# Performance work log

Measured on AMD Instinct MI355X. Metric: run time of the kernel, lower is better.

The kernel has to match this reference:

```python
import jax, jax.numpy as jnp
import numpy as np

H, D, DIM = 8, 128, 1024   # heads, dim_head, model dim (inner_dim = H*D = DIM)
QB, N = 16, 512            # 'q' and 'n' dims of the [q, n, dim] inputs


def layer_norm(x, g, b, eps=1e-5):
    mu = x.mean(-1, keepdims=True)
    var = ((x - mu) ** 2).mean(-1, keepdims=True)
    return (x - mu) / jnp.sqrt(var + eps) * g + b


def setup_inputs() -> dict:
    key = jax.random.key(0)
    ks = jax.random.split(key, 8)
    rn = lambda k, shape, s=1.0: jax.random.normal(k, shape, jnp.float32) * s
    return {
        'q': rn(ks[0], (QB, N, DIM)),
        'k': rn(ks[1], (QB, N, DIM)),
        'v': rn(ks[2], (QB, N, DIM)),
        'ln_g': jnp.ones(DIM, jnp.float32),
        'ln_b': jnp.zeros(DIM, jnp.float32),
        'w_in': rn(ks[3], (H * D, DIM), 0.02),          # Linear(dim -> inner_dim), no bias
        'wp_w1': rn(ks[4], (D, 2 * D), 0.05),           # weight_predictor Linear(2d -> d)
        'wp_b1': jnp.zeros(D, jnp.float32),
        'wp_ln_g': jnp.ones(D, jnp.float32),
        'wp_ln_b': jnp.zeros(D, jnp.float32),
        'wp_w2': rn(ks[5], (3, D), 0.05),               # Linear(d -> 3)
        'wp_b2': jnp.zeros(3, jnp.float32),
        'w_out': rn(ks[6], (DIM, H * D), 0.02),         # output Linear(inner_dim -> dim)
        'b_out': jnp.zeros(DIM, jnp.float32),
    }


def reference(q, k, v, ln_g, ln_b, w_in, wp_w1, wp_b1, wp_ln_g, wp_ln_b,
              wp_w2, wp_b2, w_out, b_out):
    def proj(t):
        x = layer_norm(t, ln_g, ln_b) @ w_in.T                 # [Q, N, H*D]
        Qd, Nd = t.shape[0], t.shape[1]
        return x.reshape(Qd, Nd, H, D).transpose(2, 0, 1, 3)   # [h, q, n, d]

    f_q, f_k, f_v = proj(q), proj(k), proj(v)

    # cosine similarity component
    dots = jnp.einsum('hqnd,hqmd->hqnm', f_q, f_k)
    qn = jnp.linalg.norm(f_q, axis=-1)                          # [h, q, n]
    kn = jnp.linalg.norm(f_k, axis=-1)                          # [h, q, m]
    cosine_sim = dots / (qn[..., :, None] * kn[..., None, :])

    q_centered = f_q - f_q.mean(-1, keepdims=True)

    # variance component (unbiased variance, clipped ratio vs target_var=1)
    q_var = jnp.var(f_q, axis=-1, ddof=1)
    k_var = jnp.var(f_k, axis=-1, ddof=1)
    q_ratio = 2.0 * jnp.minimum(q_var, 1.0) / (q_var + 1.0)
    k_ratio = 2.0 * jnp.minimum(k_var, 1.0) / (k_var + 1.0)
    var_component = jnp.einsum('hqn,hqm->hqnm', q_ratio, k_ratio)

    # decorrelation-scaled covariance component (overwrites the dead loop in the source)
    q_flat = q_centered.reshape(H, -1, D)                        # [h, q*n, d]
    feat_corr = jnp.einsum('hnd,hne->hde', q_flat, q_flat) / q_flat.shape[1]
    feat_corr = feat_corr * (1.0 - jnp.eye(D, dtype=feat_corr.dtype))
    decorr_score = jnp.linalg.norm(feat_corr, axis=(-2, -1)) / (D * D)
    decorr_scale = jnp.exp(-5.0 * decorr_score)[:, None, None, None]
    cov_component = cosine_sim * decorr_scale

    # dynamic per-head weight mixing
    q_global = f_q.mean(axis=(1, 2))                             # [h, d]
    k_global = f_k.mean(axis=(1, 2))
    feats = jnp.concatenate([q_global, k_global], axis=-1)       # [h, 2d]
    h1 = jnp.maximum(layer_norm(feats @ wp_w1.T + wp_b1, wp_ln_g, wp_ln_b), 0.0)
    weights = jax.nn.softmax(h1 @ wp_w2.T + wp_b2, axis=-1)      # [h, 3]
    cw = weights[:, 0][:, None, None, None]
    vw = weights[:, 1][:, None, None, None]
    ww = weights[:, 2][:, None, None, None]
    mixed = cw * cosine_sim + vw * cov_component + ww * var_component

    out = jnp.einsum('hqnm,hqmd->hqnd', mixed, f_v)
    out = out.transpose(1, 2, 0, 3).reshape(q.shape[0], q.shape[1], H * D)
    return out @ w_out.T + b_out
```

## Files before the change

### kernel.cpp

```cpp
#include <hip/hip_runtime.h>
#include <hip/hip_bf16.h>

typedef unsigned short u16;
typedef __attribute__((ext_vector_type(8))) short short8;
typedef __attribute__((ext_vector_type(4))) float floatx4;

#define H 8
#define D 128
#define DIM 1024
#define QB 16
#define NSEQ 512
#define R 8192

__device__ inline u16 f2b(float x) {
    union { float f; unsigned int u; } c{x};
    unsigned int lsb = (c.u >> 16) & 1;
    unsigned int r = c.u + 0x7fffu + lsb;
    return (u16)(r >> 16);
}
__device__ inline float b2f(u16 u) {
    union { unsigned int i; float f; } c;
    c.i = (unsigned int)u << 16;
    return c.f;
}

#define GLOAD_LDS16(gptr, lptr)                                                        \
    __builtin_amdgcn_global_load_lds(                                                  \
        (const __attribute__((address_space(1))) unsigned int*)(gptr),                 \
        (__attribute__((address_space(3))) unsigned int*)(lptr), 16, 0, 0)

__global__ __launch_bounds__(256) void ln_all(const float* __restrict__ q,
                                              const float* __restrict__ k,
                                              const float* __restrict__ v,
                                              const float* __restrict__ g,
                                              const float* __restrict__ b,
                                              u16* __restrict__ out) {
    const float* src = (blockIdx.y == 0) ? q : (blockIdx.y == 1) ? k : v;
    int r = blockIdx.x;
    int tid = threadIdx.x;
    const float* row = src + (size_t)r * DIM;
    float4 vv = *(const float4*)(row + tid * 4);
    float sum = vv.x + vv.y + vv.z + vv.w;
    float sq = vv.x * vv.x + vv.y * vv.y + vv.z * vv.z + vv.w * vv.w;
    __shared__ float s1[256], s2[256];
    s1[tid] = sum; s2[tid] = sq;
    __syncthreads();
    for (int s = 128; s > 0; s >>= 1) {
        if (tid < s) { s1[tid] += s1[tid + s]; s2[tid] += s2[tid + s]; }
        __syncthreads();
    }
    float mean = s1[0] * (1.0f / DIM);
    float var = s2[0] * (1.0f / DIM) - mean * mean;
    float rstd = rsqrtf(var + 1e-5f);
    float4 gv = *(const float4*)(g + tid * 4);
    float4 bv = *(const float4*)(b + tid * 4);
    ushort4 pk;
    pk.x = f2b((vv.x - mean) * rstd * gv.x + bv.x);
    pk.y = f2b((vv.y - mean) * rstd * gv.y + bv.y);
    pk.z = f2b((vv.z - mean) * rstd * gv.z + bv.z);
    pk.w = f2b((vv.w - mean) * rstd * gv.w + bv.w);
    *(ushort4*)(out + ((size_t)blockIdx.y * R + r) * DIM + tid * 4) = pk;
}

__global__ __launch_bounds__(256) void cvt2_kernel(const float* __restrict__ a,
                                                   const float* __restrict__ b,
                                                   u16* __restrict__ oa,
                                                   u16* __restrict__ ob, int n4each) {
    int i = blockIdx.x * 256 + threadIdx.x;
    const float* src; u16* dst; int j;
    if (i < n4each) { src = a; dst = oa; j = i; }
    else            { src = b; dst = ob; j = i - n4each; }
    float4 v = *(const float4*)(src + (size_t)j * 4);
    ushort4 pk;
    pk.x = f2b(v.x); pk.y = f2b(v.y); pk.z = f2b(v.z); pk.w = f2b(v.w);
    *(ushort4*)(dst + (size_t)j * 4) = pk;
}

__global__ __launch_bounds__(256) void gemm_qkv(const u16* __restrict__ A,
                                                const u16* __restrict__ B,
                                                u16* __restrict__ qT,
                                                u16* __restrict__ fqb,
                                                u16* __restrict__ kTh,
                                                u16* __restrict__ vT,
                                                float* __restrict__ qn,
                                                float* __restrict__ qm,
                                                float* __restrict__ qr,
                                                float* __restrict__ kn,
                                                float* __restrict__ kr) {
    __shared__ u16 smem[19712];
    u16* As = smem;
    u16* Bs = smem + 4096;
    float* sred = (float*)(smem + 18432);
    float* invb = (float*)(smem + 19456);

    const int tid = threadIdx.x;
    const int bb = blockIdx.x;
    const int xcd = bb & 7, j0 = bb >> 3;
    const int h = j0 & 7;
    const int rowblk = xcd * 24 + (j0 >> 3);
    const int m0 = rowblk * 128, n0 = h * 128;
    const int seg = rowblk >> 6;
    const int lrb = (rowblk & 63) * 128;

    const int wave = tid >> 6, lane = tid & 63;
    const int wm = (wave >> 1) * 64, wn = (wave & 1) * 64;
    const int fr = lane & 15, kq = lane >> 4;
    const int srow = tid >> 2, scol = (tid & 3) * 8;

    floatx4 acc[4][4] = {};
    const size_t aOff0 = (size_t)(m0 + srow) * DIM + scol;
    const size_t aOff1 = (size_t)(m0 + 64 + srow) * DIM + scol;
    const size_t bOff0 = (size_t)(n0 + srow) * DIM + scol;
    const size_t bOff1 = (size_t)(n0 + 64 + srow) * DIM + scol;

    for (int kt = 0; kt < DIM; kt += 32) {
        GLOAD_LDS16(A + aOff0 + kt, As + tid * 8);
        GLOAD_LDS16(A + aOff1 + kt, As + (256 + tid) * 8);
        GLOAD_LDS16(B + bOff0 + kt, Bs + tid * 8);
        GLOAD_LDS16(B + bOff1 + kt, Bs + (256 + tid) * 8);
        __syncthreads();
        short8 xf[4], wf[4];
#pragma unroll
        for (int i = 0; i < 4; i++)
            xf[i] = *(const short8*)&As[(wm + i * 16 + fr) * 32 + kq * 8];
#pragma unroll
        for (int j = 0; j < 4; j++)
            wf[j] = *(const short8*)&Bs[(wn + j * 16 + fr) * 32 + kq * 8];
#pragma unroll
        for (int j = 0; j < 4; j++)
#pragma unroll
            for (int i = 0; i < 4; i++)
                acc[j][i] = __builtin_amdgcn_mfma_f32_16x16x32_bf16(wf[j], xf[i], acc[j][i], 0, 0, 0);
        __syncthreads();
    }

    if (seg <= 1) {
        const int half = wn >> 6;
#pragma unroll
        for (int i = 0; i < 4; i++) {
            float s = 0.0f, qs = 0.0f;
#pragma unroll
            for (int j = 0; j < 4; j++)
#pragma unroll
                for (int rg = 0; rg < 4; rg++) {
                    float vv = acc[j][i][rg];
                    s += vv; qs += vv * vv;
                }
            s += __shfl_xor(s, 16); qs += __shfl_xor(qs, 16);
            s += __shfl_xor(s, 32); qs += __shfl_xor(qs, 32);
            if (kq == 0) {
                int rl = wm + i * 16 + fr;
                sred[rl * 4 + half * 2 + 0] = s;
                sred[rl * 4 + half * 2 + 1] = qs;
            }
        }
        __syncthreads();
        if (tid < 128) {
            float sum = sred[tid * 4 + 0] + sred[tid * 4 + 2];
            float sq  = sred[tid * 4 + 1] + sred[tid * 4 + 3];
            float nrm = sqrtf(sq);
            float var = (sq - sum * sum * (1.0f / D)) * (1.0f / (D - 1));
            float ratio = 2.0f * fminf(var, 1.0f) / (var + 1.0f);
            size_t idx = (size_t)h * R + lrb + tid;
            if (seg == 0) {
                qn[idx] = nrm; qm[idx] = sum * (1.0f / D); qr[idx] = ratio;
            } else {
                kn[idx] = nrm; kr[idx] = ratio;
                invb[tid] = 1.0f / nrm;
            }
        }
        __syncthreads();
    }

    u16* dstT = (seg == 0) ? qT : (seg == 1) ? kTh : vT;
#pragma unroll
    for (int i = 0; i < 4; i++) {
        const int rl = wm + i * 16 + fr;
        const float sc = (seg == 1) ? invb[rl] : 1.0f;
#pragma unroll
        for (int j = 0; j < 4; j++) {
#pragma unroll
            for (int rg = 0; rg < 4; rg++) {
                const int cl = wn + j * 16 + kq * 4 + rg;
                dstT[(size_t)(h * D + cl) * R + lrb + rl] = f2b(acc[j][i][rg] * sc);
            }
        }
    }

    if (seg == 0) {
        __syncthreads();
        u16* Tw = smem + wave * 4608;
#pragma unroll
        for (int i = 0; i < 4; i++)
#pragma unroll
            for (int j = 0; j < 4; j++) {
                ushort4 pk;
                pk.x = f2b(acc[j][i][0]); pk.y = f2b(acc[j][i][1]);
                pk.z = f2b(acc[j][i][2]); pk.w = f2b(acc[j][i][3]);
                *(ushort4*)&Tw[(i * 16 + fr) * 72 + j * 16 + kq * 4] = pk;
            }
        __syncthreads();
#pragma unroll
        for (int p = 0; p < 16; p++) {
            int rloc = p * 4 + kq;
            int c4 = fr * 4;
            ushort4 v = *(const ushort4*)&Tw[rloc * 72 + c4];
            *(ushort4*)&fqb[(size_t)(lrb + wm + rloc) * DIM + h * D + wn + c4] = v;
        }
    }
}

__global__ __launch_bounds__(256) void colsum2(const u16* __restrict__ qT,
                                               const u16* __restrict__ kTh,
                                               const float* __restrict__ qm,
                                               const float* __restrict__ kn,
                                               float* __restrict__ qg,
                                               float* __restrict__ kg,
                                               float* __restrict__ ubuf,
                                               float* __restrict__ s2) {
    int dg = blockIdx.x, h = blockIdx.y, mode = blockIdx.z, tid = threadIdx.x;
    const u16* fT = mode ? kTh : qT;
    const float* wvec = mode ? kn : qm;
    __shared__ float r1[256], r2[256];
    for (int dd = 0; dd < 8; dd++) {
        int d = dg * 8 + dd;
        const u16* rowp = fT + (size_t)(h * D + d) * R;
        float s = 0.0f, su = 0.0f;
        for (int it = 0; it < 32; it++) {
            int r = it * 256 + tid;
            float v = b2f(rowp[r]);
            float w = wvec[h * R + r];
            if (mode) s += v * w;
            else { s += v; su += v * w; }
        }
        r1[tid] = s; r2[tid] = su;
        __syncthreads();
        for (int st = 128; st > 0; st >>= 1) {
            if (tid < st) { r1[tid] += r1[tid + st]; r2[tid] += r2[tid + st]; }
            __syncthreads();
        }
        if (tid == 0) {
            if (mode) kg[h * D + d] = r1[0] * (1.0f / R);
            else { qg[h * D + d] = r1[0] * (1.0f / R); ubuf[h * D + d] = r2[0]; }
        }
        __syncthreads();
    }
    if (!mode && dg == 0) {
        float t = 0.0f;
        for (int it = 0; it < 32; it++) {
            float m = qm[h * R + it * 256 + tid];
            t += m * m;
        }
        r1[tid] = t;
        __syncthreads();
        for (int st = 128; st > 0; st >>= 1) {
            if (tid < st) r1[tid] += r1[tid + st];
            __syncthreads();
        }
        if (tid == 0) s2[h] = r1[0];
    }
}

__global__ __launch_bounds__(256) void syrk_q(const u16* __restrict__ qT,
                                              float* __restrict__ P) {
    __shared__ u16 As[128 * 32];
    const int c = blockIdx.x, h = blockIdx.y;
    const int tid = threadIdx.x;
    const int wave = tid >> 6, lane = tid & 63;
    const int wm = (wave >> 1) * 64, wn = (wave & 1) * 64;
    const int fr = lane & 15, kq = lane >> 4;
    const int srow = tid >> 2, scol = (tid & 3) * 8;
    floatx4 acc[4][4] = {};
    const size_t a0 = (size_t)(h * D + srow) * R + c * 256 + scol;
    const size_t a1 = (size_t)(h * D + 64 + srow) * R + c * 256 + scol;
    for (int kt = 0; kt < 256; kt += 32) {
        GLOAD_LDS16(qT + a0 + kt, As + tid * 8);
        GLOAD_LDS16(qT + a1 + kt, As + (256 + tid) * 8);
        __syncthreads();
        short8 af[4], bf[4];
#pragma unroll
        for (int i = 0; i < 4; i++)
            af[i] = *(const short8*)&As[(wm + i * 16 + fr) * 32 + kq * 8];
#pragma unroll
        for (int j = 0; j < 4; j++)
            bf[j] = *(const short8*)&As[(wn + j * 16 + fr) * 32 + kq * 8];
#pragma unroll
        for (int i = 0; i < 4; i++)
#pragma unroll
            for (int j = 0; j < 4; j++)
                acc[i][j] = __builtin_amdgcn_mfma_f32_16x16x32_bf16(af[i], bf[j], acc[i][j], 0, 0, 0);
        __syncthreads();
    }
    float* base = P + (size_t)(h * 32 + c) * (D * D);
#pragma unroll
    for (int i = 0; i < 4; i++) {
        int dr = wm + i * 16 + kq * 4;
#pragma unroll
        for (int j = 0; j < 4; j++) {
            int ec = wn + j * 16 + fr;
#pragma unroll
            for (int r = 0; r < 4; r++)
                base[(size_t)(dr + r) * D + ec] = acc[i][j][r];
        }
    }
}

__global__ __launch_bounds__(256) void decorr_sum(const float* __restrict__ P,
                                                  const float* __restrict__ ubuf,
                                                  const float* __restrict__ s2b,
                                                  float* __restrict__ Spart) {
    int bx = blockIdx.x, h = blockIdx.y, tid = threadIdx.x;
    float s2h = s2b[h];
    float S = 0.0f;
    for (int t = 0; t < 8; t++) {
        int de = bx * 2048 + t * 256 + tid;
        int dd = de >> 7, ee = de & 127;
        float g = 0.0f;
        for (int c = 0; c < 32; c++)
            g += P[(size_t)(h * 32 + c) * (D * D) + de];
        if (dd != ee) {
            float vv = (g - ubuf[h * D + dd] - ubuf[h * D + ee] + s2h) * (1.0f / R);
            S += vv * vv;
        }
    }
    __shared__ float r1[256];
    r1[tid] = S;
    __syncthreads();
    for (int st = 128; st > 0; st >>= 1) {
        if (tid < st) r1[tid] += r1[tid + st];
        __syncthreads();
    }
    if (tid == 0) Spart[h * 8 + bx] = r1[0];
}

__global__ __launch_bounds__(256) void head_kernel(const float* __restrict__ Spart,
                                                   const float* __restrict__ qg,
                                                   const float* __restrict__ kg,
                                                   const float* __restrict__ w1,
                                                   const float* __restrict__ b1,
                                                   const float* __restrict__ lng,
                                                   const float* __restrict__ lnb,
                                                   const float* __restrict__ w2,
                                                   const float* __restrict__ b2,
                                                   float* __restrict__ coef) {
    int h = blockIdx.x, tid = threadIdx.x;
    __shared__ float s1[256], s2[256], s3[256];
    __shared__ float feats[256];
    float Ssum = 0.0f;
    for (int c = 0; c < 8; c++) Ssum += Spart[h * 8 + c];
    float dscale = expf(-5.0f * sqrtf(Ssum) / (float)(D * D));
    feats[tid] = (tid < 128) ? qg[h * D + tid] : kg[h * D + tid - 128];
    __syncthreads();
    float yv = 0.0f;
    if (tid < 128) {
        float a = b1[tid];
        for (int i = 0; i < 256; i++) a = fmaf(feats[i], w1[tid * 256 + i], a);
        yv = a;
    }
    s1[tid] = (tid < 128) ? yv : 0.0f;
    s2[tid] = (tid < 128) ? yv * yv : 0.0f;
    __syncthreads();
    for (int s = 128; s > 0; s >>= 1) {
        if (tid < s) { s1[tid] += s1[tid + s]; s2[tid] += s2[tid + s]; }
        __syncthreads();
    }
    float mean = s1[0] * (1.0f / 128.0f);
    float var = s2[0] * (1.0f / 128.0f) - mean * mean;
    float rstd = rsqrtf(var + 1e-5f);
    float rel = 0.0f;
    if (tid < 128)
        rel = fmaxf((yv - mean) * rstd * lng[tid] + lnb[tid], 0.0f);
    __syncthreads();
    s1[tid] = (tid < 128) ? rel * w2[0 * 128 + tid] : 0.0f;
    s2[tid] = (tid < 128) ? rel * w2[1 * 128 + tid] : 0.0f;
    s3[tid] = (tid < 128) ? rel * w2[2 * 128 + tid] : 0.0f;
    __syncthreads();
    for (int s = 128; s > 0; s >>= 1) {
        if (tid < s) { s1[tid] += s1[tid + s]; s2[tid] += s2[tid + s]; s3[tid] += s3[tid + s]; }
        __syncthreads();
    }
    if (tid == 0) {
        float g0 = s1[0] + b2[0], g1 = s2[0] + b2[1], g2 = s3[0] + b2[2];
        float mx = fmaxf(g0, fmaxf(g1, g2));
        float e0 = expf(g0 - mx), e1 = expf(g1 - mx), e2 = expf(g2 - mx);
        float inv = 1.0f / (e0 + e1 + e2);
        coef[h * 2 + 0] = e0 * inv + e1 * inv * dscale;
        coef[h * 2 + 1] = e2 * inv;
    }
}

__global__ __launch_bounds__(256) void ktv_mfma(const u16* __restrict__ kTh,
                                                const u16* __restrict__ vT,
                                                const float* __restrict__ kr,
                                                u16* __restrict__ Mt,
                                                float* __restrict__ sv) {
    __shared__ u16 As[128 * 32];
    __shared__ u16 Bs[128 * 32];
    __shared__ float wbuf[32];
    __shared__ float svred[256];
    const int qi = blockIdx.x, h = blockIdx.y;
    const int tid = threadIdx.x;
    const int wave = tid >> 6, lane = tid & 63;
    const int wm = (wave >> 1) * 64, wn = (wave & 1) * 64;
    const int fr = lane & 15, kq = lane >> 4;
    const int srow = tid >> 2, scol = (tid & 3) * 8;
    const int m0g = qi * 512;
    const size_t a0 = (size_t)(h * D + srow) * R + m0g + scol;
    const size_t a1 = (size_t)(h * D + 64 + srow) * R + m0g + scol;
    const int e_id = tid & 127, eh = tid >> 7;
    float svacc = 0.0f;
    floatx4 acc[4][4] = {};
    for (int kt = 0; kt < 512; kt += 32) {
        GLOAD_LDS16(vT + a0 + kt, As + tid * 8);
        GLOAD_LDS16(vT + a1 + kt, As + (256 + tid) * 8);
        GLOAD_LDS16(kTh + a0 + kt, Bs + tid * 8);
        GLOAD_LDS16(kTh + a1 + kt, Bs + (256 + tid) * 8);
        if (tid < 32) wbuf[tid] = kr[(size_t)h * R + m0g + kt + tid];
        __syncthreads();
        short8 af[4], bf[4];
#pragma unroll
        for (int i = 0; i < 4; i++)
            af[i] = *(const short8*)&As[(wm + i * 16 + fr) * 32 + kq * 8];
#pragma unroll
        for (int j = 0; j < 4; j++)
            bf[j] = *(const short8*)&Bs[(wn + j * 16 + fr) * 32 + kq * 8];
#pragma unroll
        for (int i = 0; i < 4; i++)
#pragma unroll
            for (int j = 0; j < 4; j++)
                acc[i][j] = __builtin_amdgcn_mfma_f32_16x16x32_bf16(af[i], bf[j], acc[i][j], 0, 0, 0);
#pragma unroll
        for (int jm = 0; jm < 16; jm++) {
            int mm = eh * 16 + jm;
            svacc += b2f(As[e_id * 32 + mm]) * wbuf[mm];
        }
        __syncthreads();
    }
    u16* mb = Mt + (size_t)(h * QB + qi) * D * D;
#pragma unroll
    for (int i = 0; i < 4; i++) {
        int er = wm + i * 16 + kq * 4;
#pragma unroll
        for (int j = 0; j < 4; j++) {
            int dc = wn + j * 16 + fr;
#pragma unroll
            for (int r = 0; r < 4; r++)
                mb[(size_t)(er + r) * D + dc] = f2b(acc[i][j][r]);
        }
    }
    svred[tid] = svacc;
    __syncthreads();
    if (tid < 128)
        sv[(size_t)(h * QB + qi) * D + tid] = svred[tid] + svred[tid + 128];
}

__global__ __launch_bounds__(256) void attn_mfma(const u16* __restrict__ fqb,
                                                 const u16* __restrict__ Mt,
                                                 const float* __restrict__ qn,
                                                 const float* __restrict__ qr,
                                                 const float* __restrict__ sv,
                                                 const float* __restrict__ coef,
                                                 u16* __restrict__ outb) {
    __shared__ u16 As[128 * 32];
    __shared__ u16 Bs[128 * 32];
    const int nb = blockIdx.x, qi = blockIdx.y, h = blockIdx.z;
    const int tid = threadIdx.x;
    const int wave = tid >> 6, lane = tid & 63;
    const int wm = (wave >> 1) * 64, wn = (wave & 1) * 64;
    const int fr = lane & 15, kq = lane >> 4;
    const int srow = tid >> 2, scol = (tid & 3) * 8;
    const int n0g = qi * 512 + nb * 128;
    const size_t a0 = (size_t)(n0g + srow) * DIM + h * D + scol;
    const size_t a1 = (size_t)(n0g + 64 + srow) * DIM + h * D + scol;
    const u16* mtb = Mt + (size_t)(h * QB + qi) * D * D;
    floatx4 acc[4][4] = {};
    for (int kt = 0; kt < 128; kt += 32) {
        GLOAD_LDS16(fqb + a0 + kt, As + tid * 8);
        GLOAD_LDS16(fqb + a1 + kt, As + (256 + tid) * 8);
        GLOAD_LDS16(mtb + (size_t)srow * D + kt + scol, Bs + tid * 8);
        GLOAD_LDS16(mtb + (size_t)(64 + srow) * D + kt + scol, Bs + (256 + tid) * 8);
        __syncthreads();
        short8 af[4], bf[4];
#pragma unroll
        for (int i = 0; i < 4; i++)
            af[i] = *(const short8*)&As[(wm + i * 16 + fr) * 32 + kq * 8];
#pragma unroll
        for (int j = 0; j < 4; j++)
            bf[j] = *(const short8*)&Bs[(wn + j * 16 + fr) * 32 + kq * 8];
#pragma unroll
        for (int i = 0; i < 4; i++)
#pragma unroll
            for (int j = 0; j < 4; j++)
                acc[i][j] = __builtin_amdgcn_mfma_f32_16x16x32_bf16(af[i], bf[j], acc[i][j], 0, 0, 0);
        __syncthreads();
    }
    float c0 = coef[2 * h], c1 = coef[2 * h + 1];
#pragma unroll
    for (int i = 0; i < 4; i++) {
        int nr = n0g + wm + i * 16 + kq * 4;
        float sc1[4], sc2[4];
#pragma unroll
        for (int r = 0; r < 4; r++) {
            sc1[r] = c0 / qn[(size_t)h * R + nr + r];
            sc2[r] = c1 * qr[(size_t)h * R + nr + r];
        }
#pragma unroll
        for (int j = 0; j < 4; j++) {
            int ec = wn + j * 16 + fr;
            float svv = sv[(size_t)(h * QB + qi) * D + ec];
#pragma unroll
            for (int r = 0; r < 4; r++)
                outb[(size_t)(nr + r) * DIM + h * D + ec] = f2b(sc1[r] * acc[i][j][r] + sc2[r] * svv);
        }
    }
}

__global__ __launch_bounds__(256) void gemm_out(const u16* __restrict__ A,
                                                const u16* __restrict__ B,
                                                const float* __restrict__ bias,
                                                float* __restrict__ C) {
    __shared__ u16 As[128 * 32];
    __shared__ u16 Bs[128 * 32];
    const int tid = threadIdx.x;
    const int bb = blockIdx.x;
    const int xcd = bb & 7, jj = bb >> 3;
    const int col = jj & 7, rowblk = xcd * 8 + (jj >> 3);
    const int m0 = rowblk * 128, n0 = col * 128;
    const int wave = tid >> 6, lane = tid & 63;
    const int wm = (wave >> 1) * 64, wn = (wave & 1) * 64;
    const int fr = lane & 15, kq = lane >> 4;
    const int srow = tid >> 2, scol = (tid & 3) * 8;
    floatx4 acc[4][4] = {};
    const size_t aOff0 = (size_t)(m0 + srow) * DIM + scol;
    const size_t aOff1 = (size_t)(m0 + 64 + srow) * DIM + scol;
    const size_t bOff0 = (size_t)(n0 + srow) * DIM + scol;
    const size_t bOff1 = (size_t)(n0 + 64 + srow) * DIM + scol;
    for (int kt = 0; kt < DIM; kt += 32) {
        GLOAD_LDS16(A + aOff0 + kt, As + tid * 8);
        GLOAD_LDS16(A + aOff1 + kt, As + (256 + tid) * 8);
        GLOAD_LDS16(B + bOff0 + kt, Bs + tid * 8);
        GLOAD_LDS16(B + bOff1 + kt, Bs + (256 + tid) * 8);
        __syncthreads();
        short8 af[4], bf[4];
#pragma unroll
        for (int i = 0; i < 4; i++)
            af[i] = *(const short8*)&As[(wm + i * 16 + fr) * 32 + kq * 8];
#pragma unroll
        for (int j = 0; j < 4; j++)
            bf[j] = *(const short8*)&Bs[(wn + j * 16 + fr) * 32 + kq * 8];
#pragma unroll
        for (int i = 0; i < 4; i++)
#pragma unroll
            for (int j = 0; j < 4; j++)
                acc[i][j] = __builtin_amdgcn_mfma_f32_16x16x32_bf16(af[i], bf[j], acc[i][j], 0, 0, 0);
        __syncthreads();
    }
#pragma unroll
    for (int i = 0; i < 4; i++) {
        int rbase = m0 + wm + i * 16 + kq * 4;
#pragma unroll
        for (int j = 0; j < 4; j++) {
            int c = n0 + wn + j * 16 + fr;
            float badd = bias[c];
#pragma unroll
            for (int r = 0; r < 4; r++)
                C[(size_t)(rbase + r) * DIM + c] = acc[i][j][r] + badd;
        }
    }
}

extern "C" void kernel_launch(void* const* d_in, const int* in_sizes, int n_in,
                              void* d_out, int out_size, void* d_ws, size_t ws_size,
                              hipStream_t stream) {
    (void)in_sizes; (void)n_in; (void)out_size; (void)ws_size;
    const float* q      = (const float*)d_in[0];
    const float* k      = (const float*)d_in[1];
    const float* v      = (const float*)d_in[2];
    const float* ln_g   = (const float*)d_in[3];
    const float* ln_b   = (const float*)d_in[4];
    const float* w_in   = (const float*)d_in[5];
    const float* wp_w1  = (const float*)d_in[6];
    const float* wp_b1  = (const float*)d_in[7];
    const float* wp_lng = (const float*)d_in[8];
    const float* wp_lnb = (const float*)d_in[9];
    const float* wp_w2  = (const float*)d_in[10];
    const float* wp_b2  = (const float*)d_in[11];
    const float* w_out  = (const float*)d_in[12];
    const float* b_out  = (const float*)d_in[13];
    float* out = (float*)d_out;

    constexpr size_t F = (size_t)R * DIM;
    u16* lnall   = (u16*)d_ws;
    u16* fqb     = lnall + 3 * F;
    u16* qT      = fqb + F;
    u16* kTh     = qT + F;
    u16* vT      = kTh + F;
    u16* w_in16  = vT + F;
    u16* w_out16 = w_in16 + (size_t)DIM * DIM;
    u16* Mt      = w_out16 + (size_t)DIM * DIM;
    float* P     = (float*)(Mt + (size_t)H * QB * D * D);
    float* qn    = P + (size_t)32 * H * D * D;
    float* qm    = qn + (size_t)H * R;
    float* qr    = qm + (size_t)H * R;
    float* kn    = qr + (size_t)H * R;
    float* kr    = kn + (size_t)H * R;
    float* qg    = kr + (size_t)H * R;
    float* kg    = qg + H * D;
    float* ubuf  = kg + H * D;
    float* s2    = ubuf + H * D;
    float* Spart = s2 + H;
    float* coef  = Spart + H * 8;
    float* svb   = coef + 16;

    cvt2_kernel<<<2048, 256, 0, stream>>>(w_in, w_out, w_in16, w_out16, DIM * DIM / 4);
    ln_all<<<dim3(R, 3), 256, 0, stream>>>(q, k, v, ln_g, ln_b, lnall);

    gemm_qkv<<<1536, 256, 0, stream>>>(lnall, w_in16, qT, fqb, kTh, vT,
                                       qn, qm, qr, kn, kr);

    colsum2<<<dim3(16, H, 2), 256, 0, stream>>>(qT, kTh, qm, kn, qg, kg, ubuf, s2);

    syrk_q<<<dim3(32, H), 256, 0, stream>>>(qT, P);
    decorr_sum<<<dim3(8, H), 256, 0, stream>>>(P, ubuf, s2, Spart);

    head_kernel<<<H, 256, 0, stream>>>(Spart, qg, kg, wp_w1, wp_b1,
                                       wp_lng, wp_lnb, wp_w2, wp_b2, coef);

    ktv_mfma<<<dim3(QB, H), 256, 0, stream>>>(kTh, vT, kr, Mt, svb);

    attn_mfma<<<dim3(4, QB, H), 256, 0, stream>>>(fqb, Mt, qn, qr, svb, coef, lnall);

    gemm_out<<<512, 256, 0, stream>>>(lnall, w_out16, b_out, out);
}
```

Before: 344.8 us.

## Use wave-shuffle reductions, double K-step in GEMMs, vectorize loads across kernels

Replaces shared-memory tree reductions in ln_all, colsum2 and decorr_sum with wave-level shuffle reductions and a four-entry cross-wave combine, cutting the number of barriers. The QKV and output GEMMs now load two 32-wide K slices per iteration, which halves the barrier count per K loop at the cost of more LDS. colsum2, ktv_mfma and attn_mfma switch to vectorized loads. decorr_sum is spread over 32 blocks per head, with its partial sums written into the now-unused qm buffer. Reusing qm this way is safe only while nothing reads qm after colsum2.

```diff
diff --git a/kernel.cpp b/kernel.cpp
--- a/kernel.cpp
+++ b/kernel.cpp
@@ -38,19 +38,23 @@
     const float* src = (blockIdx.y == 0) ? q : (blockIdx.y == 1) ? k : v;
     int r = blockIdx.x;
     int tid = threadIdx.x;
+    const int wv = tid >> 6, lane = tid & 63;
     const float* row = src + (size_t)r * DIM;
     float4 vv = *(const float4*)(row + tid * 4);
     float sum = vv.x + vv.y + vv.z + vv.w;
     float sq = vv.x * vv.x + vv.y * vv.y + vv.z * vv.z + vv.w * vv.w;
-    __shared__ float s1[256], s2[256];
-    s1[tid] = sum; s2[tid] = sq;
+#pragma unroll
+    for (int o = 32; o > 0; o >>= 1) {
+        sum += __shfl_xor(sum, o);
+        sq  += __shfl_xor(sq, o);
+    }
+    __shared__ float s1[4], s2[4];
+    if (lane == 0) { s1[wv] = sum; s2[wv] = sq; }
     __syncthreads();
-    for (int s = 128; s > 0; s >>= 1) {
-        if (tid < s) { s1[tid] += s1[tid + s]; s2[tid] += s2[tid + s]; }
-        __syncthreads();
-    }
-    float mean = s1[0] * (1.0f / DIM);
-    float var = s2[0] * (1.0f / DIM) - mean * mean;
+    sum = s1[0] + s1[1] + s1[2] + s1[3];
+    sq  = s2[0] + s2[1] + s2[2] + s2[3];
+    float mean = sum * (1.0f / DIM);
+    float var = sq * (1.0f / DIM) - mean * mean;
     float rstd = rsqrtf(var + 1e-5f);
     float4 gv = *(const float4*)(g + tid * 4);
     float4 bv = *(const float4*)(b + tid * 4);
@@ -88,8 +92,10 @@
                                                 float* __restrict__ kn,
                                                 float* __restrict__ kr) {
     __shared__ u16 smem[19712];
-    u16* As = smem;
-    u16* Bs = smem + 4096;
+    u16* As  = smem;
+    u16* Bs  = smem + 4096;
+    u16* As2 = smem + 8192;
+    u16* Bs2 = smem + 12288;
     float* sred = (float*)(smem + 18432);
     float* invb = (float*)(smem + 19456);
 
@@ -113,11 +119,15 @@
     const size_t bOff0 = (size_t)(n0 + srow) * DIM + scol;
     const size_t bOff1 = (size_t)(n0 + 64 + srow) * DIM + scol;
 
-    for (int kt = 0; kt < DIM; kt += 32) {
+    for (int kt = 0; kt < DIM; kt += 64) {
         GLOAD_LDS16(A + aOff0 + kt, As + tid * 8);
         GLOAD_LDS16(A + aOff1 + kt, As + (256 + tid) * 8);
         GLOAD_LDS16(B + bOff0 + kt, Bs + tid * 8);
         GLOAD_LDS16(B + bOff1 + kt, Bs + (256 + tid) * 8);
+        GLOAD_LDS16(A + aOff0 + kt + 32, As2 + tid * 8);
+        GLOAD_LDS16(A + aOff1 + kt + 32, As2 + (256 + tid) * 8);
+        GLOAD_LDS16(B + bOff0 + kt + 32, Bs2 + tid * 8);
+        GLOAD_LDS16(B + bOff1 + kt + 32, Bs2 + (256 + tid) * 8);
         __syncthreads();
         short8 xf[4], wf[4];
 #pragma unroll
@@ -131,6 +141,18 @@
 #pragma unroll
             for (int i = 0; i < 4; i++)
                 acc[j][i] = __builtin_amdgcn_mfma_f32_16x16x32_bf16(wf[j], xf[i], acc[j][i], 0, 0, 0);
+        short8 xg[4], wg[4];
+#pragma unroll
+        for (int i = 0; i < 4; i++)
+            xg[i] = *(const short8*)&As2[(wm + i * 16 + fr) * 32 + kq * 8];
+#pragma unroll
+        for (int j = 0; j < 4; j++)
+            wg[j] = *(const short8*)&Bs2[(wn + j * 16 + fr) * 32 + kq * 8];
+#pragma unroll
+        for (int j = 0; j < 4; j++)
+#pragma unroll
+            for (int i = 0; i < 4; i++)
+                acc[j][i] = __builtin_amdgcn_mfma_f32_16x16x32_bf16(wg[j], xg[i], acc[j][i], 0, 0, 0);
         __syncthreads();
     }
 
@@ -221,43 +243,51 @@
     int dg = blockIdx.x, h = blockIdx.y, mode = blockIdx.z, tid = threadIdx.x;
     const u16* fT = mode ? kTh : qT;
     const float* wvec = mode ? kn : qm;
-    __shared__ float r1[256], r2[256];
+    const int wv = tid >> 6, lane = tid & 63;
+    __shared__ float red[2][4];
+    const float* wp = wvec + (size_t)h * R;
     for (int dd = 0; dd < 8; dd++) {
         int d = dg * 8 + dd;
         const u16* rowp = fT + (size_t)(h * D + d) * R;
         float s = 0.0f, su = 0.0f;
-        for (int it = 0; it < 32; it++) {
-            int r = it * 256 + tid;
-            float v = b2f(rowp[r]);
-            float w = wvec[h * R + r];
-            if (mode) s += v * w;
-            else { s += v; su += v * w; }
-        }
-        r1[tid] = s; r2[tid] = su;
-        __syncthreads();
-        for (int st = 128; st > 0; st >>= 1) {
-            if (tid < st) { r1[tid] += r1[tid + st]; r2[tid] += r2[tid + st]; }
-            __syncthreads();
-        }
+        for (int it = 0; it < 8; it++) {
+            int r = it * 1024 + tid * 4;
+            uint2 pv = *(const uint2*)(rowp + r);
+            float4 w = *(const float4*)(wp + r);
+            float v0 = b2f((u16)(pv.x & 0xffffu)), v1 = b2f((u16)(pv.x >> 16));
+            float v2 = b2f((u16)(pv.y & 0xffffu)), v3 = b2f((u16)(pv.y >> 16));
+            if (mode) s += v0 * w.x + v1 * w.y + v2 * w.z + v3 * w.w;
+            else {
+                s += v0 + v1 + v2 + v3;
+                su += v0 * w.x + v1 * w.y + v2 * w.z + v3 * w.w;
+            }
+        }
+#pragma unroll
+        for (int o = 32; o > 0; o >>= 1) {
+            s += __shfl_xor(s, o);
+            su += __shfl_xor(su, o);
+        }
+        if (lane == 0) { red[0][wv] = s; red[1][wv] = su; }
+        __syncthreads();
         if (tid == 0) {
-            if (mode) kg[h * D + d] = r1[0] * (1.0f / R);
-            else { qg[h * D + d] = r1[0] * (1.0f / R); ubuf[h * D + d] = r2[0]; }
+            float S  = red[0][0] + red[0][1] + red[0][2] + red[0][3];
+            float SU = red[1][0] + red[1][1] + red[1][2] + red[1][3];
+            if (mode) kg[h * D + d] = S * (1.0f / R);
+            else { qg[h * D + d] = S * (1.0f / R); ubuf[h * D + d] = SU; }
         }
         __syncthreads();
     }
     if (!mode && dg == 0) {
         float t = 0.0f;
-        for (int it = 0; it < 32; it++) {
-            float m = qm[h * R + it * 256 + tid];
-            t += m * m;
-        }
-        r1[tid] = t;
-        __syncthreads();
-        for (int st = 128; st > 0; st >>= 1) {
-            if (tid < st) r1[tid] += r1[tid + st];
-            __syncthreads();
-        }
-        if (tid == 0) s2[h] = r1[0];
+        for (int it = 0; it < 8; it++) {
+            float4 m4 = *(const float4*)(qm + (size_t)h * R + it * 1024 + tid * 4);
+            t += m4.x * m4.x + m4.y * m4.y + m4.z * m4.z + m4.w * m4.w;
+        }
+#pragma unroll
+        for (int o = 32; o > 0; o >>= 1) t += __shfl_xor(t, o);
+        if (lane == 0) red[0][wv] = t;
+        __syncthreads();
+        if (tid == 0) s2[h] = red[0][0] + red[0][1] + red[0][2] + red[0][3];
     }
 }
 
@@ -312,8 +342,8 @@
     int bx = blockIdx.x, h = blockIdx.y, tid = threadIdx.x;
     float s2h = s2b[h];
     float S = 0.0f;
-    for (int t = 0; t < 8; t++) {
-        int de = bx * 2048 + t * 256 + tid;
+    for (int t = 0; t < 2; t++) {
+        int de = bx * 512 + t * 256 + tid;
         int dd = de >> 7, ee = de & 127;
         float g = 0.0f;
         for (int c = 0; c < 32; c++)
@@ -323,14 +353,12 @@
             S += vv * vv;
         }
     }
-    __shared__ float r1[256];
-    r1[tid] = S;
+#pragma unroll
+    for (int o = 32; o > 0; o >>= 1) S += __shfl_xor(S, o);
+    __shared__ float r1[4];
+    if ((tid & 63) == 0) r1[tid >> 6] = S;
     __syncthreads();
-    for (int st = 128; st > 0; st >>= 1) {
-        if (tid < st) r1[tid] += r1[tid + st];
-        __syncthreads();
-    }
-    if (tid == 0) Spart[h * 8 + bx] = r1[0];
+    if (tid == 0) Spart[h * 32 + bx] = r1[0] + r1[1] + r1[2] + r1[3];
 }
 
 __global__ __launch_bounds__(256) void head_kernel(const float* __restrict__ Spart,
@@ -347,7 +375,7 @@
     __shared__ float s1[256], s2[256], s3[256];
     __shared__ float feats[256];
     float Ssum = 0.0f;
-    for (int c = 0; c < 8; c++) Ssum += Spart[h * 8 + c];
+    for (int c = 0; c < 32; c++) Ssum += Spart[h * 32 + c];
     float dscale = expf(-5.0f * sqrtf(Ssum) / (float)(D * D));
     feats[tid] = (tid < 128) ? qg[h * D + tid] : kg[h * D + tid - 128];
     __syncthreads();
@@ -407,7 +435,7 @@
     const int m0g = qi * 512;
     const size_t a0 = (size_t)(h * D + srow) * R + m0g + scol;
     const size_t a1 = (size_t)(h * D + 64 + srow) * R + m0g + scol;
-    const int e_id = tid & 127, eh = tid >> 7;
+    const int e_id = tid & 127, eh = tid >> 7, mb16 = (tid >> 7) * 16;
     float svacc = 0.0f;
     floatx4 acc[4][4] = {};
     for (int kt = 0; kt < 512; kt += 32) {
@@ -429,13 +457,19 @@
 #pragma unroll
             for (int j = 0; j < 4; j++)
                 acc[i][j] = __builtin_amdgcn_mfma_f32_16x16x32_bf16(af[i], bf[j], acc[i][j], 0, 0, 0);
-#pragma unroll
-        for (int jm = 0; jm < 16; jm++) {
-            int mm = eh * 16 + jm;
-            svacc += b2f(As[e_id * 32 + mm]) * wbuf[mm];
-        }
-        __syncthreads();
-    }
+        {
+            short8 va = *(const short8*)&As[e_id * 32 + mb16];
+            short8 vb = *(const short8*)&As[e_id * 32 + mb16 + 8];
+#pragma unroll
+            for (int jm = 0; jm < 8; jm++)
+                svacc += b2f((u16)va[jm]) * wbuf[mb16 + jm];
+#pragma unroll
+            for (int jm = 0; jm < 8; jm++)
+                svacc += b2f((u16)vb[jm]) * wbuf[mb16 + 8 + jm];
+        }
+        __syncthreads();
+    }
+    (void)eh;
     u16* mb = Mt + (size_t)(h * QB + qi) * D * D;
 #pragma unroll
     for (int i = 0; i < 4; i++) {
@@ -498,12 +532,10 @@
 #pragma unroll
     for (int i = 0; i < 4; i++) {
         int nr = n0g + wm + i * 16 + kq * 4;
-        float sc1[4], sc2[4];
-#pragma unroll
-        for (int r = 0; r < 4; r++) {
-            sc1[r] = c0 / qn[(size_t)h * R + nr + r];
-            sc2[r] = c1 * qr[(size_t)h * R + nr + r];
-        }
+        float4 nv = *(const float4*)&qn[(size_t)h * R + nr];
+        float4 rv = *(const float4*)&qr[(size_t)h * R + nr];
+        float sc1[4] = {c0 / nv.x, c0 / nv.y, c0 / nv.z, c0 / nv.w};
+        float sc2[4] = {c1 * rv.x, c1 * rv.y, c1 * rv.z, c1 * rv.w};
 #pragma unroll
         for (int j = 0; j < 4; j++) {
             int ec = wn + j * 16 + fr;
@@ -519,8 +551,8 @@
                                                 const u16* __restrict__ B,
                                                 const float* __restrict__ bias,
                                                 float* __restrict__ C) {
-    __shared__ u16 As[128 * 32];
-    __shared__ u16 Bs[128 * 32];
+    __shared__ u16 As[128 * 64];
+    __shared__ u16 Bs[128 * 64];
     const int tid = threadIdx.x;
     const int bb = blockIdx.x;
     const int xcd = bb & 7, jj = bb >> 3;
@@ -535,11 +567,15 @@
     const size_t aOff1 = (size_t)(m0 + 64 + srow) * DIM + scol;
     const size_t bOff0 = (size_t)(n0 + srow) * DIM + scol;
     const size_t bOff1 = (size_t)(n0 + 64 + srow) * DIM + scol;
-    for (int kt = 0; kt < DIM; kt += 32) {
+    for (int kt = 0; kt < DIM; kt += 64) {
         GLOAD_LDS16(A + aOff0 + kt, As + tid * 8);
         GLOAD_LDS16(A + aOff1 + kt, As + (256 + tid) * 8);
+        GLOAD_LDS16(A + aOff0 + kt + 32, As + (512 + tid) * 8);
+        GLOAD_LDS16(A + aOff1 + kt + 32, As + (768 + tid) * 8);
         GLOAD_LDS16(B + bOff0 + kt, Bs + tid * 8);
         GLOAD_LDS16(B + bOff1 + kt, Bs + (256 + tid) * 8);
+        GLOAD_LDS16(B + bOff0 + kt + 32, Bs + (512 + tid) * 8);
+        GLOAD_LDS16(B + bOff1 + kt + 32, Bs + (768 + tid) * 8);
         __syncthreads();
         short8 af[4], bf[4];
 #pragma unroll
@@ -553,6 +589,18 @@
 #pragma unroll
             for (int j = 0; j < 4; j++)
                 acc[i][j] = __builtin_amdgcn_mfma_f32_16x16x32_bf16(af[i], bf[j], acc[i][j], 0, 0, 0);
+        short8 ag[4], bg[4];
+#pragma unroll
+        for (int i = 0; i < 4; i++)
+            ag[i] = *(const short8*)&As[4096 + (wm + i * 16 + fr) * 32 + kq * 8];
+#pragma unroll
+        for (int j = 0; j < 4; j++)
+            bg[j] = *(const short8*)&Bs[4096 + (wn + j * 16 + fr) * 32 + kq * 8];
+#pragma unroll
+        for (int i = 0; i < 4; i++)
+#pragma unroll
+            for (int j = 0; j < 4; j++)
+                acc[i][j] = __builtin_amdgcn_mfma_f32_16x16x32_bf16(ag[i], bg[j], acc[i][j], 0, 0, 0);
         __syncthreads();
     }
 #pragma unroll
@@ -611,6 +659,7 @@
     float* Spart = s2 + H;
     float* coef  = Spart + H * 8;
     float* svb   = coef + 16;
+    float* SpartN = qm;
 
     cvt2_kernel<<<2048, 256, 0, stream>>>(w_in, w_out, w_in16, w_out16, DIM * DIM / 4);
     ln_all<<<dim3(R, 3), 256, 0, stream>>>(q, k, v, ln_g, ln_b, lnall);
@@ -621,9 +670,9 @@
     colsum2<<<dim3(16, H, 2), 256, 0, stream>>>(qT, kTh, qm, kn, qg, kg, ubuf, s2);
 
     syrk_q<<<dim3(32, H), 256, 0, stream>>>(qT, P);
-    decorr_sum<<<dim3(8, H), 256, 0, stream>>>(P, ubuf, s2, Spart);
-
-    head_kernel<<<H, 256, 0, stream>>>(Spart, qg, kg, wp_w1, wp_b1,
+    decorr_sum<<<dim3(32, H), 256, 0, stream>>>(P, ubuf, s2, SpartN);
+
+    head_kernel<<<H, 256, 0, stream>>>(SpartN, qg, kg, wp_w1, wp_b1,
                                        wp_lng, wp_lnb, wp_w2, wp_b2, coef);
 
     ktv_mfma<<<dim3(QB, H), 256, 0, stream>>>(kTh, vT, kr, Mt, svb);
```

New measurement: 338.4 us. Within noise of the previous version (-1.9%).
